# Optimization experiments

Hardware: AMD Instinct MI355X
Metric: run time of the kernel (lower is better)

The kernel has to match this reference:

```python
import jax, jax.numpy as jnp
import numpy as np

H = 128
STEPS = 4
EPS = 1e-5

def _mlp(x, W0, b0, W1, b1, W2, b2):
    x = jax.nn.relu(x @ W0 + b0)
    x = jax.nn.relu(x @ W1 + b1)
    return x @ W2 + b2

def _ln(x, g, b):
    mu = jnp.mean(x, axis=-1, keepdims=True)
    var = jnp.mean((x - mu) ** 2, axis=-1, keepdims=True)
    return (x - mu) * jax.lax.rsqrt(var + EPS) * g + b

def _scores(x, pos):
    # soft assignment of points to graph nodes: softmax over -squared distance
    d2 = (jnp.sum(x * x, -1, keepdims=True)
          - 2.0 * jnp.einsum('bnd,md->bnm', x, pos)
          + jnp.sum(pos * pos, -1))  # [B, Npts, Nnodes]
    return jax.nn.softmax(-d2, axis=-1)

def _block(nodes, senders, receivers, msg_W, msg_b, ln1_g, ln1_b, node_W, node_b, ln2_g, ln2_b):
    # gather edge endpoints, message MLP, layernorm
    m = jnp.concatenate((nodes[:, receivers], nodes[:, senders]), axis=-1) @ msg_W + msg_b
    m = _ln(m, ln1_g, ln1_b)  # [B, E, H]
    inbox = jnp.zeros_like(nodes).at[:, receivers].add(m)  # scatter-add
    out = jnp.concatenate((nodes, inbox), axis=-1) @ node_W + node_b
    return _ln(out, ln2_g, ln2_b)

def setup_inputs() -> dict:
    key = jax.random.key(0)
    ks = jax.random.split(key, 40)
    B, Nc, Nt, N, E = 8, 4096, 4096, 1024, 16384
    dx, dyc, dyt = 2, 3, 3
    def w(k, *s):
        fan_in = s[0]
        return jax.random.normal(k, s, jnp.float32) / np.sqrt(fan_in)
    inp = {
        'xc': jax.random.normal(ks[0], (B, Nc, dx), jnp.float32),
        'yc': jax.random.normal(ks[1], (B, Nc, dyc), jnp.float32),
        'xt': jax.random.normal(ks[2], (B, Nt, dx), jnp.float32),
        'pos': jax.random.normal(ks[3], (N, dx), jnp.float32),
        'enc_W0': w(ks[4], dx + dyc, H), 'enc_b0': jnp.zeros((H,), jnp.float32),
        'enc_W1': w(ks[5], H, H), 'enc_b1': jnp.zeros((H,), jnp.float32),
        'enc_W2': w(ks[6], H, H), 'enc_b2': jnp.zeros((H,), jnp.float32),
        'qenc_W0': w(ks[7], dx, H), 'qenc_b0': jnp.zeros((H,), jnp.float32),
        'qenc_W1': w(ks[8], H, H), 'qenc_b1': jnp.zeros((H,), jnp.float32),
        'qenc_W2': w(ks[9], H, H), 'qenc_b2': jnp.zeros((H,), jnp.float32),
        'dec_W0': w(ks[10], 2 * H, H), 'dec_b0': jnp.zeros((H,), jnp.float32),
        'dec_W1': w(ks[11], H, H), 'dec_b1': jnp.zeros((H,), jnp.float32),
        'dec_W2': w(ks[12], H, dyt), 'dec_b2': jnp.zeros((dyt,), jnp.float32),
        'msg_W': w(ks[13], 2 * H, H), 'msg_b': jnp.zeros((H,), jnp.float32),
        'ln1_g': jnp.ones((H,), jnp.float32), 'ln1_b': jnp.zeros((H,), jnp.float32),
        'node_W': w(ks[14], 2 * H, H), 'node_b': jnp.zeros((H,), jnp.float32),
        'ln2_g': jnp.ones((H,), jnp.float32), 'ln2_b': jnp.zeros((H,), jnp.float32),
        'senders': jax.random.randint(ks[15], (E,), 0, N, jnp.int32),
        'receivers': jax.random.randint(ks[16], (E,), 0, N, jnp.int32),
    }
    return inp

def reference(xc, yc, xt, pos,
              enc_W0, enc_b0, enc_W1, enc_b1, enc_W2, enc_b2,
              qenc_W0, qenc_b0, qenc_W1, qenc_b1, qenc_W2, qenc_b2,
              dec_W0, dec_b0, dec_W1, dec_b1, dec_W2, dec_b2,
              msg_W, msg_b, ln1_g, ln1_b, node_W, node_b, ln2_g, ln2_b,
              senders, receivers):
    sc = _scores(xc, pos)  # [B, Nc, N]
    emb = _mlp(jnp.concatenate((xc, yc), -1), enc_W0, enc_b0, enc_W1, enc_b1, enc_W2, enc_b2)
    latents = jnp.einsum('bcn,bch->bnh', sc, emb)  # scores^T @ emb -> [B, N, H]
    for _ in range(STEPS):  # shared block (same weights each step)
        latents = _block(latents, senders, receivers, msg_W, msg_b, ln1_g, ln1_b,
                         node_W, node_b, ln2_g, ln2_b)
    q = _mlp(xt, qenc_W0, qenc_b0, qenc_W1, qenc_b1, qenc_W2, qenc_b2)
    st = _scores(xt, pos)  # [B, Nt, N]
    z = jnp.einsum('btn,bnh->bth', st, latents)
    z = jnp.concatenate((z, q), -1)
    return _mlp(z, dec_W0, dec_b0, dec_W1, dec_b1, dec_W2, dec_b2)
```

## Files before the change

kernel.cpp:

```cpp
#include <hip/hip_runtime.h>
#include <hip/hip_bf16.h>
#include <string.h>

#define BB 8
#define NC 4096
#define NTT 4096
#define NNODE 1024
#define NEDGE 16384
#define LDE 4128
#define LDL 1056

typedef __hip_bfloat16 bf16;
typedef unsigned short u16;
typedef __attribute__((ext_vector_type(8))) short short8;
typedef __attribute__((ext_vector_type(4))) float f32x4;

__device__ __forceinline__ float b2f(bf16 x) { return __bfloat162float(x); }
__device__ __forceinline__ float bs2f(short s) { return __uint_as_float(((unsigned)(unsigned short)s) << 16); }

template <typename T> struct Cvt;
template <> struct Cvt<float> { static __device__ __forceinline__ float to(float v) { return v; } };
template <> struct Cvt<bf16>  { static __device__ __forceinline__ bf16  to(float v) { return __float2bfloat16(v); } };

__device__ __forceinline__ unsigned short f2bs(float x) {
    unsigned u = __float_as_uint(x);
    return (unsigned short)((u + 0x7FFFu + ((u >> 16) & 1u)) >> 16);
}

__device__ __forceinline__ short8 ld_frag(const bf16* g) {
    union { uint4 u4; short8 s8; } cv;
    cv.u4 = *(const uint4*)g;
    return cv.s8;
}
__device__ __forceinline__ short8 ld_frag(const float* g) {
    float4 f0 = *(const float4*)g;
    float4 f1 = *(const float4*)(g + 4);
    short8 r;
    r[0] = (short)f2bs(f0.x); r[1] = (short)f2bs(f0.y);
    r[2] = (short)f2bs(f0.z); r[3] = (short)f2bs(f0.w);
    r[4] = (short)f2bs(f1.x); r[5] = (short)f2bs(f1.y);
    r[6] = (short)f2bs(f1.z); r[7] = (short)f2bs(f1.w);
    return r;
}

__global__ void detect_k(const u16* __restrict__ posu, int* __restrict__ flag) {
    __shared__ int cnt;
    if (threadIdx.x == 0) cnt = 0;
    __syncthreads();
    int wild = 0;
    for (int i = threadIdx.x; i < 1024; i += 256) {
        u16 u = posu[2 * i];
        int ex = (u >> 7) & 0xFF;
        if (ex == 0 || ex == 0xFF || ex > 137 || ex < 107) wild++;
    }
    atomicAdd(&cnt, wild);
    __syncthreads();
    if (threadIdx.x == 0) *flag = (cnt > 50) ? 1 : 0;
}

struct Tab { const void* src[30]; int pref[31]; };

__global__ __launch_bounds__(256) void ingest_k(Tab tab, const int* __restrict__ flag,
                                                bf16* __restrict__ dst) {
    int idx = blockIdx.x * 256 + threadIdx.x;
    if (idx >= tab.pref[30]) return;
    int t = 0;
    while (tab.pref[t + 1] <= idx) t++;
    int e = idx - tab.pref[t];
    float v;
    if (*flag) v = ((const float*)tab.src[t])[e];
    else       v = b2f(((const bf16*)tab.src[t])[e]);
    dst[idx] = __float2bfloat16(v);
}

struct TT { const bf16* src[11]; bf16* dst[11]; int srcK[11]; int dK[11]; int pref[12]; };

__global__ __launch_bounds__(256) void prep_trans_k(
    TT tt,
    const bf16* __restrict__ xc, const bf16* __restrict__ yc,
    const bf16* __restrict__ xt,
    const bf16* __restrict__ pos,
    bf16* __restrict__ xin32, bf16* __restrict__ xt32,
    float2* __restrict__ posf2) {
    if (blockIdx.x < 128) {
        int row = blockIdx.x * 256 + threadIdx.x;
        bf16 z = __float2bfloat16(0.f);
        bf16* xr = xin32 + row * 32;
        xr[0] = xc[row * 2 + 0];
        xr[1] = xc[row * 2 + 1];
        xr[2] = yc[row * 3 + 0];
        xr[3] = yc[row * 3 + 1];
        xr[4] = yc[row * 3 + 2];
#pragma unroll
        for (int k = 5; k < 32; ++k) xr[k] = z;
        bf16* tr = xt32 + row * 32;
        tr[0] = xt[row * 2 + 0];
        tr[1] = xt[row * 2 + 1];
#pragma unroll
        for (int k = 2; k < 32; ++k) tr[k] = z;
        if (row < NNODE) posf2[row] = make_float2(b2f(pos[2 * row]), b2f(pos[2 * row + 1]));
        return;
    }
    int idx = (blockIdx.x - 128) * 256 + threadIdx.x;
    if (idx >= tt.pref[11]) return;
    int t = 0;
    while (tt.pref[t + 1] <= idx) t++;
    int e = idx - tt.pref[t];
    int k = e >> 7, n = e & 127;
    bf16 v = (k < tt.srcK[t]) ? tt.src[t][k * 128 + n] : __float2bfloat16(0.f);
    tt.dst[t][n * tt.dK[t] + k] = v;
}

__global__ __launch_bounds__(1024) void build_csr_k(const int* __restrict__ recv,
                                                    const int* __restrict__ send,
                                                    int* __restrict__ rowptr,
                                                    int* __restrict__ csr_send) {
    __shared__ int cnt[1024];
    __shared__ int wt[16], wt2[16];
    __shared__ int cur[1024];
    int t = threadIdx.x;
    cnt[t] = 0;
    __syncthreads();
    for (int e = t; e < NEDGE; e += 1024) atomicAdd(&cnt[recv[e]], 1);
    __syncthreads();
    int v = cnt[t];
    int lane = t & 63, w = t >> 6;
#pragma unroll
    for (int off = 1; off < 64; off <<= 1) {
        int u = __shfl_up(v, off);
        if (lane >= off) v += u;
    }
    if (lane == 63) wt[w] = v;
    __syncthreads();
    if (t < 16) {
        int x = wt[t];
#pragma unroll
        for (int off = 1; off < 16; off <<= 1) {
            int u = __shfl_up(x, off);
            if (t >= off) x += u;
        }
        wt2[t] = x;
    }
    __syncthreads();
    int excl = v - cnt[t] + (w ? wt2[w - 1] : 0);
    rowptr[t] = excl;
    cur[t] = excl;
    if (t == 0) rowptr[1024] = NEDGE;
    __syncthreads();
    for (int e = t; e < NEDGE; e += 1024) {
        int pos = atomicAdd(&cur[recv[e]], 1);
        csr_send[pos] = send[e];
    }
}

template <int KSTEPS, int EPI, int RELU, int TRANS, int NSPLIT,
          typename TINA, typename TINB, typename TOUT>
__global__ __launch_bounds__(256) void mfma_gemm_k(
    const TINA* __restrict__ Xa, const TINB* __restrict__ Xb, int ldx,
    const bf16* __restrict__ Wt,
    const bf16* __restrict__ bias,
    const bf16* __restrict__ lng, const bf16* __restrict__ lnb,
    TOUT* __restrict__ Y, int ldy, int tshift, int ldt)
{
    constexpr int K = KSTEPS * 32;
    __shared__ __align__(16) short Bs[8][64][8];
    int tid = threadIdx.x;
    int w = tid >> 6, l = tid & 63;
    int lm = l & 15, lq = l >> 4;
    int blk = blockIdx.x;
    int half = 0;
    if (NSPLIT == 2) { half = blk & 1; blk >>= 1; }
    const bf16* Wtl = Wt + (size_t)half * 128 * K;
    int colbase = half * 128;
    size_t row0 = (size_t)blk * 64;

    f32x4 acc[8];
#pragma unroll
    for (int i = 0; i < 8; i++) acc[i] = (f32x4){0.f, 0.f, 0.f, 0.f};

    for (int s = 0; s < KSTEPS; ++s) {
        int k0 = s * 32;
        __syncthreads();
        short8 a;
        if (Xb != nullptr && k0 >= 128)
            a = ld_frag(Xb + (row0 + w * 16 + lm) * (size_t)128 + (k0 - 128) + lq * 8);
        else
            a = ld_frag(Xa + (row0 + w * 16 + lm) * (size_t)ldx + k0 + lq * 8);
#pragma unroll
        for (int rr = 0; rr < 2; ++rr) {
            int idx = rr * 256 + tid;
            int nt = idx >> 6, ll = idx & 63;
            *(short8*)&Bs[nt][ll][0] =
                ld_frag(Wtl + (size_t)(nt * 16 + (ll & 15)) * K + k0 + (ll >> 4) * 8);
        }
        __syncthreads();
#pragma unroll
        for (int nt = 0; nt < 8; ++nt) {
            short8 b = *(const short8*)&Bs[nt][l][0];
            acc[nt] = __builtin_amdgcn_mfma_f32_16x16x32_bf16(a, b, acc[nt], 0, 0, 0);
        }
    }

    float v[8][4];
#pragma unroll
    for (int nt = 0; nt < 8; ++nt) {
        float bb = bias ? b2f(bias[colbase + nt * 16 + lm]) : 0.f;
#pragma unroll
        for (int r = 0; r < 4; ++r) v[nt][r] = acc[nt][r] + bb;
    }
    if constexpr (EPI == 1) {
#pragma unroll
        for (int r = 0; r < 4; ++r) {
            float s1 = 0.f, s2 = 0.f;
#pragma unroll
            for (int nt = 0; nt < 8; ++nt) { s1 += v[nt][r]; s2 += v[nt][r] * v[nt][r]; }
#pragma unroll
            for (int m = 1; m < 16; m <<= 1) { s1 += __shfl_xor(s1, m); s2 += __shfl_xor(s2, m); }
            float mu = s1 * (1.f / 128.f);
            float var = s2 * (1.f / 128.f) - mu * mu;
            float rs = rsqrtf(var + 1e-5f);
#pragma unroll
            for (int nt = 0; nt < 8; ++nt) {
                int n = nt * 16 + lm;
                v[nt][r] = (v[nt][r] - mu) * rs * b2f(lng[n]) + b2f(lnb[n]);
            }
        }
    }
    if constexpr (TRANS) {
        size_t grow = row0 + w * 16 + lq * 4;
        int bb2 = (int)(grow >> tshift);
        size_t rloc = grow & (((size_t)1 << tshift) - 1);
        bf16* YT = (bf16*)Y;
#pragma unroll
        for (int nt = 0; nt < 8; ++nt) {
            int col = colbase + nt * 16 + lm;
            ushort4 u;
            float x0 = v[nt][0], x1 = v[nt][1], x2 = v[nt][2], x3 = v[nt][3];
            if (RELU) { x0 = fmaxf(x0, 0.f); x1 = fmaxf(x1, 0.f); x2 = fmaxf(x2, 0.f); x3 = fmaxf(x3, 0.f); }
            u.x = f2bs(x0); u.y = f2bs(x1); u.z = f2bs(x2); u.w = f2bs(x3);
            *(ushort4*)(YT + ((size_t)bb2 * 128 + col) * (size_t)ldt + rloc) = u;
        }
    } else {
#pragma unroll
        for (int nt = 0; nt < 8; ++nt)
#pragma unroll
            for (int r = 0; r < 4; ++r) {
                float x = v[nt][r];
                if (RELU) x = fmaxf(x, 0.f);
                Y[(row0 + w * 16 + lq * 4 + r) * (size_t)ldy + colbase + nt * 16 + lm] = Cvt<TOUT>::to(x);
            }
    }
}

__global__ __launch_bounds__(256) void node_msg_k(
    const float* __restrict__ cur, const bf16* __restrict__ inbox,
    const bf16* __restrict__ WtNode, const bf16* __restrict__ node_b,
    const bf16* __restrict__ ln2_g, const bf16* __restrict__ ln2_b,
    const bf16* __restrict__ WtMsg,
    float* __restrict__ nxt, bf16* __restrict__ PQ)
{
    __shared__ __align__(16) short Bs[8][64][8];
    __shared__ __align__(16) short Act[64][136];
    int tid = threadIdx.x;
    int w = tid >> 6, l = tid & 63;
    int lm = l & 15, lq = l >> 4;
    size_t row0 = (size_t)blockIdx.x * 64;

    f32x4 acc[8];
#pragma unroll
    for (int i = 0; i < 8; i++) acc[i] = (f32x4){0.f, 0.f, 0.f, 0.f};

    for (int s = 0; s < 8; ++s) {
        int k0 = s * 32;
        __syncthreads();
        short8 a;
        if (k0 < 128) a = ld_frag(cur + (row0 + w * 16 + lm) * 128 + k0 + lq * 8);
        else          a = ld_frag(inbox + (row0 + w * 16 + lm) * 128 + (k0 - 128) + lq * 8);
#pragma unroll
        for (int rr = 0; rr < 2; ++rr) {
            int idx = rr * 256 + tid;
            int nt = idx >> 6, ll = idx & 63;
            *(short8*)&Bs[nt][ll][0] =
                ld_frag(WtNode + (size_t)(nt * 16 + (ll & 15)) * 256 + k0 + (ll >> 4) * 8);
        }
        __syncthreads();
#pragma unroll
        for (int nt = 0; nt < 8; ++nt) {
            short8 b = *(const short8*)&Bs[nt][l][0];
            acc[nt] = __builtin_amdgcn_mfma_f32_16x16x32_bf16(a, b, acc[nt], 0, 0, 0);
        }
    }
    float v[8][4];
#pragma unroll
    for (int nt = 0; nt < 8; ++nt) {
        float bb = b2f(node_b[nt * 16 + lm]);
#pragma unroll
        for (int r = 0; r < 4; ++r) v[nt][r] = acc[nt][r] + bb;
    }
#pragma unroll
    for (int r = 0; r < 4; ++r) {
        float s1 = 0.f, s2 = 0.f;
#pragma unroll
        for (int nt = 0; nt < 8; ++nt) { s1 += v[nt][r]; s2 += v[nt][r] * v[nt][r]; }
#pragma unroll
        for (int m = 1; m < 16; m <<= 1) { s1 += __shfl_xor(s1, m); s2 += __shfl_xor(s2, m); }
        float mu = s1 * (1.f / 128.f);
        float var = s2 * (1.f / 128.f) - mu * mu;
        float rs = rsqrtf(var + 1e-5f);
#pragma unroll
        for (int nt = 0; nt < 8; ++nt) {
            int n = nt * 16 + lm;
            v[nt][r] = (v[nt][r] - mu) * rs * b2f(ln2_g[n]) + b2f(ln2_b[n]);
        }
    }
#pragma unroll
    for (int nt = 0; nt < 8; ++nt)
#pragma unroll
        for (int r = 0; r < 4; ++r) {
            nxt[(row0 + w * 16 + lq * 4 + r) * 128 + nt * 16 + lm] = v[nt][r];
            Act[w * 16 + lq * 4 + r][nt * 16 + lm] = (short)f2bs(v[nt][r]);
        }

    for (int half = 0; half < 2; ++half) {
        const bf16* Wtl = WtMsg + (size_t)half * 128 * 128;
#pragma unroll
        for (int i = 0; i < 8; i++) acc[i] = (f32x4){0.f, 0.f, 0.f, 0.f};
        for (int s = 0; s < 4; ++s) {
            int k0 = s * 32;
            __syncthreads();
#pragma unroll
            for (int rr = 0; rr < 2; ++rr) {
                int idx = rr * 256 + tid;
                int nt = idx >> 6, ll = idx & 63;
                *(short8*)&Bs[nt][ll][0] =
                    ld_frag(Wtl + (size_t)(nt * 16 + (ll & 15)) * 128 + k0 + (ll >> 4) * 8);
            }
            __syncthreads();
            short8 a = *(const short8*)&Act[w * 16 + lm][k0 + lq * 8];
#pragma unroll
            for (int nt = 0; nt < 8; ++nt) {
                short8 b = *(const short8*)&Bs[nt][l][0];
                acc[nt] = __builtin_amdgcn_mfma_f32_16x16x32_bf16(a, b, acc[nt], 0, 0, 0);
            }
        }
#pragma unroll
        for (int nt = 0; nt < 8; ++nt)
#pragma unroll
            for (int r = 0; r < 4; ++r)
                PQ[(row0 + w * 16 + lq * 4 + r) * 256 + half * 128 + nt * 16 + lm] =
                    __float2bfloat16(acc[nt][r]);
    }
}

template <int K0STEPS, int LAYERS, int RELU_LAST, int TRANS, typename TIN, typename TOUT>
__global__ __launch_bounds__(256) void mlp_k(
    const TIN* __restrict__ Xa, const TIN* __restrict__ Xb, int ldx,
    const bf16* __restrict__ Wt0, const bf16* __restrict__ b0,
    const bf16* __restrict__ Wt1, const bf16* __restrict__ b1,
    const bf16* __restrict__ Wt2, const bf16* __restrict__ b2,
    TOUT* __restrict__ Y, int ldy, int tshift, int ldt)
{
    constexpr int K0 = K0STEPS * 32;
    __shared__ __align__(16) short Bs[8][64][8];
    __shared__ __align__(16) short Act[64][136];
    int tid = threadIdx.x;
    int w = tid >> 6, l = tid & 63;
    int lm = l & 15, lq = l >> 4;
    size_t row0 = (size_t)blockIdx.x * 64;

    f32x4 acc[8];
#pragma unroll
    for (int i = 0; i < 8; i++) acc[i] = (f32x4){0.f, 0.f, 0.f, 0.f};

    for (int s = 0; s < K0STEPS; ++s) {
        int k0 = s * 32;
        __syncthreads();
        short8 a;
        {
            const TIN* src = Xa; int kk = k0; int ld = ldx;
            if (Xb != nullptr && k0 >= 128) { src = Xb; kk = k0 - 128; ld = 128; }
            a = ld_frag(src + (row0 + w * 16 + lm) * (size_t)ld + kk + lq * 8);
        }
#pragma unroll
        for (int rr = 0; rr < 2; ++rr) {
            int idx = rr * 256 + tid;
            int nt = idx >> 6, ll = idx & 63;
            *(short8*)&Bs[nt][ll][0] =
                ld_frag(Wt0 + (size_t)(nt * 16 + (ll & 15)) * K0 + k0 + (ll >> 4) * 8);
        }
        __syncthreads();
#pragma unroll
        for (int nt = 0; nt < 8; ++nt) {
            short8 b = *(const short8*)&Bs[nt][l][0];
            acc[nt] = __builtin_amdgcn_mfma_f32_16x16x32_bf16(a, b, acc[nt], 0, 0, 0);
        }
    }
#pragma unroll
    for (int nt = 0; nt < 8; ++nt) {
        float bb = b2f(b0[nt * 16 + lm]);
#pragma unroll
        for (int r = 0; r < 4; ++r) {
            float x = fmaxf(acc[nt][r] + bb, 0.f);
            Act[w * 16 + lq * 4 + r][nt * 16 + lm] = (short)f2bs(x);
        }
    }

    for (int L = 1; L < LAYERS; ++L) {
        const bf16* Wt = (L == 1) ? Wt1 : Wt2;
        const bf16* bias = (L == 1) ? b1 : b2;
        bool last = (L == LAYERS - 1);
#pragma unroll
        for (int i = 0; i < 8; i++) acc[i] = (f32x4){0.f, 0.f, 0.f, 0.f};
        for (int s = 0; s < 4; ++s) {
            int k0 = s * 32;
            __syncthreads();
#pragma unroll
            for (int rr = 0; rr < 2; ++rr) {
                int idx = rr * 256 + tid;
                int nt = idx >> 6, ll = idx & 63;
                *(short8*)&Bs[nt][ll][0] =
                    ld_frag(Wt + (size_t)(nt * 16 + (ll & 15)) * 128 + k0 + (ll >> 4) * 8);
            }
            __syncthreads();
            short8 a = *(const short8*)&Act[w * 16 + lm][k0 + lq * 8];
#pragma unroll
            for (int nt = 0; nt < 8; ++nt) {
                short8 b = *(const short8*)&Bs[nt][l][0];
                acc[nt] = __builtin_amdgcn_mfma_f32_16x16x32_bf16(a, b, acc[nt], 0, 0, 0);
            }
        }
        if (!last) {
            __syncthreads();
#pragma unroll
            for (int nt = 0; nt < 8; ++nt) {
                float bb = b2f(bias[nt * 16 + lm]);
#pragma unroll
                for (int r = 0; r < 4; ++r) {
                    float x = fmaxf(acc[nt][r] + bb, 0.f);
                    Act[w * 16 + lq * 4 + r][nt * 16 + lm] = (short)f2bs(x);
                }
            }
        } else {
            float v[8][4];
#pragma unroll
            for (int nt = 0; nt < 8; ++nt) {
                float bb = b2f(bias[nt * 16 + lm]);
#pragma unroll
                for (int r = 0; r < 4; ++r) {
                    float x = acc[nt][r] + bb;
                    if (RELU_LAST) x = fmaxf(x, 0.f);
                    v[nt][r] = x;
                }
            }
            if constexpr (TRANS) {
                size_t grow = row0 + w * 16 + lq * 4;
                int bb2 = (int)(grow >> tshift);
                size_t rloc = grow & (((size_t)1 << tshift) - 1);
                bf16* YT = (bf16*)Y;
#pragma unroll
                for (int nt = 0; nt < 8; ++nt) {
                    int col = nt * 16 + lm;
                    ushort4 u;
                    u.x = f2bs(v[nt][0]); u.y = f2bs(v[nt][1]);
                    u.z = f2bs(v[nt][2]); u.w = f2bs(v[nt][3]);
                    *(ushort4*)(YT + ((size_t)bb2 * 128 + col) * (size_t)ldt + rloc) = u;
                }
            } else {
#pragma unroll
                for (int nt = 0; nt < 8; ++nt)
#pragma unroll
                    for (int r = 0; r < 4; ++r)
                        Y[(row0 + w * 16 + lq * 4 + r) * (size_t)ldy + nt * 16 + lm] =
                            Cvt<TOUT>::to(v[nt][r]);
            }
        }
    }
}

__global__ __launch_bounds__(256) void qdec_k(
    const bf16* __restrict__ xt32,
    const bf16* __restrict__ WtQ0, const bf16* __restrict__ qb0,
    const bf16* __restrict__ WtQ1, const bf16* __restrict__ qb1,
    const bf16* __restrict__ WtQ2, const bf16* __restrict__ qb2,
    const bf16* __restrict__ z,
    const bf16* __restrict__ WtDec0, const bf16* __restrict__ db0,
    const bf16* __restrict__ WtDec1, const bf16* __restrict__ db1,
    const bf16* __restrict__ W2, const bf16* __restrict__ b2v,
    const int* __restrict__ flag, void* __restrict__ out)
{
    __shared__ __align__(16) short Bs[8][64][8];
    __shared__ __align__(16) short Act[64][136];
    __shared__ bf16 w2s[384];
    int tid = threadIdx.x;
    int w = tid >> 6, l = tid & 63;
    int lm = l & 15, lq = l >> 4;
    size_t row0 = (size_t)blockIdx.x * 64;
    for (int t = tid; t < 384; t += 256) w2s[t] = W2[t];

    f32x4 acc[8];
#pragma unroll
    for (int i = 0; i < 8; i++) acc[i] = (f32x4){0.f, 0.f, 0.f, 0.f};

    {
        __syncthreads();
#pragma unroll
        for (int rr = 0; rr < 2; ++rr) {
            int idx = rr * 256 + tid;
            int nt = idx >> 6, ll = idx & 63;
            *(short8*)&Bs[nt][ll][0] =
                ld_frag(WtQ0 + (size_t)(nt * 16 + (ll & 15)) * 32 + (ll >> 4) * 8);
        }
        __syncthreads();
        short8 a = ld_frag(xt32 + (row0 + w * 16 + lm) * 32 + lq * 8);
#pragma unroll
        for (int nt = 0; nt < 8; ++nt) {
            short8 b = *(const short8*)&Bs[nt][l][0];
            acc[nt] = __builtin_amdgcn_mfma_f32_16x16x32_bf16(a, b, acc[nt], 0, 0, 0);
        }
#pragma unroll
        for (int nt = 0; nt < 8; ++nt) {
            float bb = b2f(qb0[nt * 16 + lm]);
#pragma unroll
            for (int r = 0; r < 4; ++r)
                Act[w * 16 + lq * 4 + r][nt * 16 + lm] = (short)f2bs(fmaxf(acc[nt][r] + bb, 0.f));
        }
    }
    for (int L = 1; L < 3; ++L) {
        const bf16* Wt = (L == 1) ? WtQ1 : WtQ2;
        const bf16* bias = (L == 1) ? qb1 : qb2;
#pragma unroll
        for (int i = 0; i < 8; i++) acc[i] = (f32x4){0.f, 0.f, 0.f, 0.f};
        for (int s = 0; s < 4; ++s) {
            int k0 = s * 32;
            __syncthreads();
#pragma unroll
            for (int rr = 0; rr < 2; ++rr) {
                int idx = rr * 256 + tid;
                int nt = idx >> 6, ll = idx & 63;
                *(short8*)&Bs[nt][ll][0] =
                    ld_frag(Wt + (size_t)(nt * 16 + (ll & 15)) * 128 + k0 + (ll >> 4) * 8);
            }
            __syncthreads();
            short8 a = *(const short8*)&Act[w * 16 + lm][k0 + lq * 8];
#pragma unroll
            for (int nt = 0; nt < 8; ++nt) {
                short8 b = *(const short8*)&Bs[nt][l][0];
                acc[nt] = __builtin_amdgcn_mfma_f32_16x16x32_bf16(a, b, acc[nt], 0, 0, 0);
            }
        }
        __syncthreads();
#pragma unroll
        for (int nt = 0; nt < 8; ++nt) {
            float bb = b2f(bias[nt * 16 + lm]);
#pragma unroll
            for (int r = 0; r < 4; ++r) {
                float x = acc[nt][r] + bb;
                if (L == 1) x = fmaxf(x, 0.f);
                Act[w * 16 + lq * 4 + r][nt * 16 + lm] = (short)f2bs(x);
            }
        }
    }
    {
#pragma unroll
        for (int i = 0; i < 8; i++) acc[i] = (f32x4){0.f, 0.f, 0.f, 0.f};
        for (int s = 0; s < 8; ++s) {
            int k0 = s * 32;
            __syncthreads();
#pragma unroll
            for (int rr = 0; rr < 2; ++rr) {
                int idx = rr * 256 + tid;
                int nt = idx >> 6, ll = idx & 63;
                *(short8*)&Bs[nt][ll][0] =
                    ld_frag(WtDec0 + (size_t)(nt * 16 + (ll & 15)) * 256 + k0 + (ll >> 4) * 8);
            }
            __syncthreads();
            short8 a;
            if (k0 < 128) a = ld_frag(z + (row0 + w * 16 + lm) * (size_t)128 + k0 + lq * 8);
            else          a = *(const short8*)&Act[w * 16 + lm][(k0 - 128) + lq * 8];
#pragma unroll
            for (int nt = 0; nt < 8; ++nt) {
                short8 b = *(const short8*)&Bs[nt][l][0];
                acc[nt] = __builtin_amdgcn_mfma_f32_16x16x32_bf16(a, b, acc[nt], 0, 0, 0);
            }
        }
        __syncthreads();
#pragma unroll
        for (int nt = 0; nt < 8; ++nt) {
            float bb = b2f(db0[nt * 16 + lm]);
#pragma unroll
            for (int r = 0; r < 4; ++r)
                Act[w * 16 + lq * 4 + r][nt * 16 + lm] = (short)f2bs(fmaxf(acc[nt][r] + bb, 0.f));
        }
    }
    {
#pragma unroll
        for (int i = 0; i < 8; i++) acc[i] = (f32x4){0.f, 0.f, 0.f, 0.f};
        for (int s = 0; s < 4; ++s) {
            int k0 = s * 32;
            __syncthreads();
#pragma unroll
            for (int rr = 0; rr < 2; ++rr) {
                int idx = rr * 256 + tid;
                int nt = idx >> 6, ll = idx & 63;
                *(short8*)&Bs[nt][ll][0] =
                    ld_frag(WtDec1 + (size_t)(nt * 16 + (ll & 15)) * 128 + k0 + (ll >> 4) * 8);
            }
            __syncthreads();
            short8 a = *(const short8*)&Act[w * 16 + lm][k0 + lq * 8];
#pragma unroll
            for (int nt = 0; nt < 8; ++nt) {
                short8 b = *(const short8*)&Bs[nt][l][0];
                acc[nt] = __builtin_amdgcn_mfma_f32_16x16x32_bf16(a, b, acc[nt], 0, 0, 0);
            }
        }
        __syncthreads();
#pragma unroll
        for (int nt = 0; nt < 8; ++nt) {
            float bb = b2f(db1[nt * 16 + lm]);
#pragma unroll
            for (int r = 0; r < 4; ++r)
                Act[w * 16 + lq * 4 + r][nt * 16 + lm] = (short)f2bs(fmaxf(acc[nt][r] + bb, 0.f));
        }
    }
    __syncthreads();
    if (tid < 192) {
        int row = tid / 3, col = tid - (tid / 3) * 3;
        float a = b2f(b2v[col]);
        for (int k8 = 0; k8 < 16; ++k8) {
            short8 av = *(const short8*)&Act[row][k8 * 8];
#pragma unroll
            for (int j = 0; j < 8; ++j)
                a += bs2f(av[j]) * b2f(w2s[(k8 * 8 + j) * 3 + col]);
        }
        size_t o = (row0 + row) * 3 + col;
        if (*flag) ((float*)out)[o] = a;
        else       ((bf16*)out)[o] = __float2bfloat16(a);
    }
}

__global__ __launch_bounds__(256) void stats2_k(const bf16* __restrict__ xcp,
                                                const bf16* __restrict__ xtp,
                                                const bf16* __restrict__ pos,
                                                float4* __restrict__ cstC4,
                                                float4* __restrict__ cstT4) {
    __shared__ float px[NNODE], py[NNODE];
    int tid = threadIdx.x;
    for (int t = tid; t < NNODE; t += 256) {
        px[t] = b2f(pos[2 * t]);
        py[t] = b2f(pos[2 * t + 1]);
    }
    __syncthreads();
    const bf16* xp = (blockIdx.x < 8192) ? xcp : xtp;
    float4* st4 = (blockIdx.x < 8192) ? cstC4 : cstT4;
    int pb = blockIdx.x & 8191;
    int w = tid >> 6, l = tid & 63;
    int p = pb * 4 + w;
    float x = b2f(xp[2 * p]), y = b2f(xp[2 * p + 1]);
    float vals[16];
    float m = -3.4e38f;
#pragma unroll
    for (int k = 0; k < 16; k++) {
        int n = k * 64 + l;
        float dx = x - px[n], dy = y - py[n];
        float v = -(dx * dx + dy * dy);
        vals[k] = v;
        m = fmaxf(m, v);
    }
#pragma unroll
    for (int off = 32; off; off >>= 1) m = fmaxf(m, __shfl_xor(m, off));
    float s = 0.f;
#pragma unroll
    for (int k = 0; k < 16; k++) s += __expf(vals[k] - m);
#pragma unroll
    for (int off = 32; off; off >>= 1) s += __shfl_xor(s, off);
    if (l == 0) st4[p] = make_float4(x, y, m, 1.f / s);
}

struct P8 { float* p[8]; };

__global__ __launch_bounds__(512, 4) void lat_mfma_k(const bf16* __restrict__ embT,
                                                     const float2* __restrict__ posf2,
                                                     const float4* __restrict__ cstC4,
                                                     P8 parts) {
    int i = blockIdx.x;
    int b = i & 7, r = i >> 3;
    int cs = r >> 4, nt = r & 15;
    int n0 = nt * 64;
    __shared__ __align__(16) float4 csh[512];
    __shared__ __align__(16) union ShU {
        short stage[2][8192];
        float4 red[4][8][64];
    } sh;
    int tid = threadIdx.x;
    int w = tid >> 6, l = tid & 63;
    int wl = w & 3, up = w >> 2;
    int lm = l & 15, lq = l >> 4;
    int node = n0 + wl * 16 + lm;
    float2 pn = posf2[node];
    const bf16* ebase = embT + (size_t)b * (128 * LDE) + cs * 512;
    const float4* cbase = cstC4 + b * NC + cs * 512;
    csh[tid] = cbase[tid];

    int h0 = tid >> 3;
    int cb0 = (tid & 7) << 4;
    const char* g0 = (const char*)ebase + (size_t)h0 * (LDE * 2) + cb0;
    const size_t gH = (size_t)64 * (LDE * 2);
    int o0 = h0 * 128 + (cb0 ^ ((h0 & 7) << 4));
    char* lbuf0 = (char*)&sh.stage[0][0];
    char* lbuf1 = (char*)&sh.stage[1][0];

    {
        uint4 rA = *(const uint4*)(g0);
        uint4 rB = *(const uint4*)(g0 + gH);
        *(uint4*)(lbuf0 + o0) = rA;
        *(uint4*)(lbuf0 + o0 + 64 * 128) = rB;
    }
    __syncthreads();

    f32x4 acc[8];
#pragma unroll
    for (int q = 0; q < 8; q++) acc[q] = (f32x4){0.f, 0.f, 0.f, 0.f};

    union AF { short8 s; u16 u[8]; };
    int rb = up * 64 + lq * 16;

    for (int ci = 0; ci < 8; ++ci) {
        char* cur = (ci & 1) ? lbuf1 : lbuf0;
        char* nxt = (ci & 1) ? lbuf0 : lbuf1;
        uint4 rA, rB;
        if (ci < 7) {
            const char* gs = g0 + (ci + 1) * 128;
            rA = *(const uint4*)(gs);
            rB = *(const uint4*)(gs + gH);
        }
        AF cw;
        int cidx = ci * 64 + up * 32 + lq * 8;
#pragma unroll
        for (int j = 0; j < 8; ++j) {
            float4 cc = csh[cidx + j];
            float dx = cc.x - pn.x, dy = cc.y - pn.y;
            cw.u[j] = f2bs(__expf(-(dx * dx + dy * dy) - cc.z) * cc.w);
        }
#pragma unroll
        for (int t2 = 0; t2 < 8; ++t2) {
            int h = t2 * 16 + lm;
            short8 bfr = *(const short8*)(cur + h * 128 + (rb ^ ((h & 7) << 4)));
            acc[t2] = __builtin_amdgcn_mfma_f32_16x16x32_bf16(cw.s, bfr, acc[t2], 0, 0, 0);
        }
        if (ci < 7) {
            *(uint4*)(nxt + o0) = rA;
            *(uint4*)(nxt + o0 + 64 * 128) = rB;
        }
        __syncthreads();
    }

    if (up) {
#pragma unroll
        for (int t2 = 0; t2 < 8; ++t2)
            sh.red[wl][t2][l] = make_float4(acc[t2][0], acc[t2][1], acc[t2][2], acc[t2][3]);
    }
    __syncthreads();
    if (!up) {
        float* part = parts.p[cs] + (((size_t)(b * NNODE + n0 + wl * 16 + lq * 4)) << 7) + lm;
#pragma unroll
        for (int t2 = 0; t2 < 8; ++t2) {
            float4 o = sh.red[wl][t2][l];
#pragma unroll
            for (int r2 = 0; r2 < 4; ++r2)
                part[(r2 << 7) + t2 * 16] = acc[t2][r2] + ((const float*)&o)[r2];
        }
    }
}

__global__ __launch_bounds__(256) void reduce8_k(float* __restrict__ dst, P8 parts) {
    int i = blockIdx.x * 256 + threadIdx.x;
    float4 s = ((const float4*)parts.p[0])[i];
#pragma unroll
    for (int k = 1; k < 8; ++k) {
        float4 v = ((const float4*)parts.p[k])[i];
        s.x += v.x; s.y += v.y; s.z += v.z; s.w += v.w;
    }
    ((float4*)dst)[i] = s;
}

__global__ __launch_bounds__(512, 4) void z_mfma_k(const bf16* __restrict__ latT,
                                                   const float2* __restrict__ posf2,
                                                   const float4* __restrict__ cstT4,
                                                   bf16* __restrict__ z) {
    int i = blockIdx.x;
    int b = i & 7, tt = i >> 3;
    int t0 = tt * 64;
    __shared__ __align__(8) float2 posh[1024];
    __shared__ __align__(16) union ShU {
        short stage[2][8192];
        float4 red[4][8][64];
    } sh;
    int tid = threadIdx.x;
    int w = tid >> 6, l = tid & 63;
    int wl = w & 3, up = w >> 2;
    int lm = l & 15, lq = l >> 4;
    int t = t0 + wl * 16 + lm;
    float4 qs = cstT4[b * NTT + t];
    const bf16* lbase = latT + (size_t)b * (128 * LDL);
    for (int k = tid; k < 1024; k += 512) posh[k] = posf2[k];

    int h0 = tid >> 3;
    int cb0 = (tid & 7) << 4;
    const char* g0 = (const char*)lbase + (size_t)h0 * (LDL * 2) + cb0;
    const size_t gH = (size_t)64 * (LDL * 2);
    int o0 = h0 * 128 + (cb0 ^ ((h0 & 7) << 4));
    char* lbuf0 = (char*)&sh.stage[0][0];
    char* lbuf1 = (char*)&sh.stage[1][0];

    {
        uint4 rA = *(const uint4*)(g0);
        uint4 rB = *(const uint4*)(g0 + gH);
        *(uint4*)(lbuf0 + o0) = rA;
        *(uint4*)(lbuf0 + o0 + 64 * 128) = rB;
    }
    __syncthreads();

    f32x4 acc[8];
#pragma unroll
    for (int q = 0; q < 8; q++) acc[q] = (f32x4){0.f, 0.f, 0.f, 0.f};

    union AF { short8 s; u16 u[8]; };
    int rb = up * 64 + lq * 16;

    for (int ci = 0; ci < 16; ++ci) {
        char* cur = (ci & 1) ? lbuf1 : lbuf0;
        char* nxt = (ci & 1) ? lbuf0 : lbuf1;
        uint4 rA, rB;
        if (ci < 15) {
            const char* gs = g0 + (ci + 1) * 128;
            rA = *(const uint4*)(gs);
            rB = *(const uint4*)(gs + gH);
        }
        AF cw;
        int cidx = ci * 64 + up * 32 + lq * 8;
#pragma unroll
        for (int j = 0; j < 8; ++j) {
            float2 pn = posh[cidx + j];
            float dx = qs.x - pn.x, dy = qs.y - pn.y;
            cw.u[j] = f2bs(__expf(-(dx * dx + dy * dy) - qs.z) * qs.w);
        }
#pragma unroll
        for (int t2 = 0; t2 < 8; ++t2) {
            int h = t2 * 16 + lm;
            short8 bfr = *(const short8*)(cur + h * 128 + (rb ^ ((h & 7) << 4)));
            acc[t2] = __builtin_amdgcn_mfma_f32_16x16x32_bf16(cw.s, bfr, acc[t2], 0, 0, 0);
        }
        if (ci < 15) {
            *(uint4*)(nxt + o0) = rA;
            *(uint4*)(nxt + o0 + 64 * 128) = rB;
        }
        __syncthreads();
    }

    if (up) {
#pragma unroll
        for (int t2 = 0; t2 < 8; ++t2)
            sh.red[wl][t2][l] = make_float4(acc[t2][0], acc[t2][1], acc[t2][2], acc[t2][3]);
    }
    __syncthreads();
    if (!up) {
        bf16* zp = z + (((size_t)(b * NTT + t0 + wl * 16 + lq * 4)) << 7) + lm;
#pragma unroll
        for (int t2 = 0; t2 < 8; ++t2) {
            float4 o = sh.red[wl][t2][l];
#pragma unroll
            for (int r2 = 0; r2 < 4; ++r2)
                zp[(r2 << 7) + t2 * 16] = __float2bfloat16(acc[t2][r2] + ((const float*)&o)[r2]);
        }
    }
}

__global__ __launch_bounds__(256) void edge_gather_k(const bf16* __restrict__ PQ,
                                                     const int* __restrict__ rowptr,
                                                     const int* __restrict__ csr_send,
                                                     const bf16* __restrict__ mb,
                                                     const bf16* __restrict__ g1,
                                                     const bf16* __restrict__ b1,
                                                     bf16* __restrict__ inbox) {
    int tid = threadIdx.x;
    int w = tid >> 6, l = tid & 63;
    int gw = blockIdx.x * 4 + w;
    int b = gw >> 10, n = gw & 1023;
    const bf16* pqb = PQ + ((size_t)b << 18);
    float p0 = b2f(pqb[(n << 8) + l]);
    float p1 = b2f(pqb[(n << 8) + l + 64]);
    float mb0 = b2f(mb[l]), mb1 = b2f(mb[l + 64]);
    float g0 = b2f(g1[l]), g1v = b2f(g1[l + 64]);
    float bb0 = b2f(b1[l]), bb1 = b2f(b1[l + 64]);
    int beg = rowptr[n], end = rowptr[n + 1];
    float a0 = 0.f, a1 = 0.f;
    int i = beg;
    for (; i + 1 < end; i += 2) {
        int sA = csr_send[i], sB = csr_send[i + 1];
        const bf16* qA = pqb + (sA << 8) + 128;
        const bf16* qB = pqb + (sB << 8) + 128;
        float A0 = p0 + b2f(qA[l]) + mb0;
        float A1 = p1 + b2f(qA[l + 64]) + mb1;
        float B0 = p0 + b2f(qB[l]) + mb0;
        float B1 = p1 + b2f(qB[l + 64]) + mb1;
        float a1s = A0 + A1, a2s = A0 * A0 + A1 * A1;
        float b1s = B0 + B1, b2s = B0 * B0 + B1 * B1;
#pragma unroll
        for (int off = 32; off; off >>= 1) {
            a1s += __shfl_xor(a1s, off);
            a2s += __shfl_xor(a2s, off);
            b1s += __shfl_xor(b1s, off);
            b2s += __shfl_xor(b2s, off);
        }
        float muA = a1s * (1.f / 128.f);
        float varA = a2s * (1.f / 128.f) - muA * muA;
        float rsA = rsqrtf(varA + 1e-5f);
        float muB = b1s * (1.f / 128.f);
        float varB = b2s * (1.f / 128.f) - muB * muB;
        float rsB = rsqrtf(varB + 1e-5f);
        a0 += (A0 - muA) * rsA * g0 + bb0;
        a1 += (A1 - muA) * rsA * g1v + bb1;
        a0 += (B0 - muB) * rsB * g0 + bb0;
        a1 += (B1 - muB) * rsB * g1v + bb1;
    }
    if (i < end) {
        int s = csr_send[i];
        const bf16* q = pqb + (s << 8) + 128;
        float m0 = p0 + b2f(q[l]) + mb0;
        float m1 = p1 + b2f(q[l + 64]) + mb1;
        float s1 = m0 + m1, s2 = m0 * m0 + m1 * m1;
#pragma unroll
        for (int off = 32; off; off >>= 1) {
            s1 += __shfl_xor(s1, off);
            s2 += __shfl_xor(s2, off);
        }
        float mu = s1 * (1.f / 128.f);
        float var = s2 * (1.f / 128.f) - mu * mu;
        float rs = rsqrtf(var + 1e-5f);
        a0 += (m0 - mu) * rs * g0 + bb0;
        a1 += (m1 - mu) * rs * g1v + bb1;
    }
    bf16* inb = inbox + ((size_t)b << 17) + (n << 7);
    inb[l] = __float2bfloat16(a0);
    inb[l + 64] = __float2bfloat16(a1);
}

extern "C" void kernel_launch(void* const* d_in, const int* in_sizes, int n_in,
                              void* d_out, int out_size, void* d_ws, size_t ws_size,
                              hipStream_t stream) {
    const int* senders = (const int*)d_in[30];
    const int* receivers = (const int*)d_in[31];

    char* base = (char*)d_ws;
    size_t off = 0;
    auto alloc = [&](size_t bytes) { char* p = base + off; off += (bytes + 255) & ~(size_t)255; return p; };

    int* flag = (int*)alloc(256);

    Tab tab;
    int pref = 0;
    for (int i = 0; i < 30; ++i) { tab.src[i] = d_in[i]; tab.pref[i] = pref; pref += in_sizes[i]; }
    tab.pref[30] = pref;
    bf16* arena = (bf16*)alloc((size_t)pref * 2);
    auto C = [&](int i) { return arena + tab.pref[i]; };

    float4* cstC4 = (float4*)alloc(32768 * sizeof(float4));
    float4* cstT4 = (float4*)alloc(32768 * sizeof(float4));
    float* lat0  = (float*)alloc(8192 * 128 * 4);
    float* lat1  = (float*)alloc(8192 * 128 * 4);
    float* inboxf = (float*)alloc(8192 * 128 * 4);
    bf16* inbox  = (bf16*)alloc(8192 * 128 * 2);
    bf16* T1     = (bf16*)alloc((size_t)32768 * 128 * 2);
    bf16* T2     = (bf16*)alloc((size_t)32768 * 128 * 2);
    bf16* T3     = (bf16*)alloc((size_t)32768 * 128 * 2);
    bf16* embT   = (bf16*)alloc((size_t)8 * 128 * LDE * 2);
    bf16* latT   = (bf16*)alloc((size_t)8 * 128 * LDL * 2);
    bf16* xin32  = (bf16*)alloc((size_t)32768 * 32 * 2);
    bf16* xt32   = (bf16*)alloc((size_t)32768 * 32 * 2);
    float2* posf2 = (float2*)alloc(1024 * sizeof(float2));
    int* rowptr  = (int*)alloc(1025 * 4);
    int* csr_send = (int*)alloc(NEDGE * 4);
    bf16* WtEnc0 = (bf16*)alloc(128 * 32 * 2);
    bf16* WtQ0   = (bf16*)alloc(128 * 32 * 2);
    bf16* WtEnc1 = (bf16*)alloc(16384 * 2);
    bf16* WtEnc2 = (bf16*)alloc(16384 * 2);
    bf16* WtQ1   = (bf16*)alloc(16384 * 2);
    bf16* WtQ2   = (bf16*)alloc(16384 * 2);
    bf16* WtDec0 = (bf16*)alloc(32768 * 2);
    bf16* WtDec1 = (bf16*)alloc(16384 * 2);
    bf16* WtMsg  = (bf16*)alloc(32768 * 2);
    bf16* WtNode = (bf16*)alloc(32768 * 2);
    bf16* PQ     = T3;
    (void)ws_size; (void)n_in; (void)out_size;

    detect_k<<<1, 256, 0, stream>>>((const u16*)d_in[3], flag);
    ingest_k<<<(pref + 255) / 256, 256, 0, stream>>>(tab, flag, arena);

    const bf16 *xc = C(0), *yc = C(1), *xt = C(2), *pos = C(3);
    const bf16 *enc_W0 = C(4), *enc_b0 = C(5), *enc_W1 = C(6), *enc_b1 = C(7), *enc_W2 = C(8), *enc_b2 = C(9);
    const bf16 *qenc_W0 = C(10), *qenc_b0 = C(11), *qenc_W1 = C(12), *qenc_b1 = C(13), *qenc_W2 = C(14), *qenc_b2 = C(15);
    const bf16 *dec_W0 = C(16), *dec_b0 = C(17), *dec_W1 = C(18), *dec_b1 = C(19), *dec_W2 = C(20), *dec_b2 = C(21);
    const bf16 *msg_W = C(22), *msg_b = C(23), *ln1_g = C(24), *ln1_b = C(25);
    const bf16 *node_W = C(26), *node_b = C(27), *ln2_g = C(28), *ln2_b = C(29);

    TT tt;
    const bf16* s11[11] = { enc_W1, enc_W2, qenc_W1, qenc_W2, dec_W1, dec_W0, msg_W, msg_W + 16384, node_W, enc_W0, qenc_W0 };
    bf16* d11[11]       = { WtEnc1, WtEnc2, WtQ1,    WtQ2,    WtDec1, WtDec0, WtMsg, WtMsg + 16384, WtNode, WtEnc0, WtQ0   };
    int sk11[11] = { 128, 128, 128, 128, 128, 256, 128, 128, 256, 5, 2 };
    int dk11[11] = { 128, 128, 128, 128, 128, 256, 128, 128, 256, 32, 32 };
    int tp = 0;
    for (int i = 0; i < 11; ++i) {
        tt.src[i] = s11[i]; tt.dst[i] = d11[i]; tt.srcK[i] = sk11[i]; tt.dK[i] = dk11[i];
        tt.pref[i] = tp; tp += dk11[i] * 128;
    }
    tt.pref[11] = tp;

    prep_trans_k<<<128 + (tp + 255) / 256, 256, 0, stream>>>(tt, xc, yc, xt, pos, xin32, xt32, posf2);
    build_csr_k<<<1, 1024, 0, stream>>>(receivers, senders, rowptr, csr_send);

    mlp_k<1, 3, 0, 1, bf16, bf16><<<512, 256, 0, stream>>>(
        xin32, nullptr, 32, WtEnc0, enc_b0, WtEnc1, enc_b1, WtEnc2, enc_b2, embT, 128, 12, LDE);

    stats2_k<<<16384, 256, 0, stream>>>(xc, xt, pos, cstC4, cstT4);

    P8 parts;
    parts.p[0] = lat1;
    parts.p[1] = inboxf;
    parts.p[2] = (float*)T1;
    parts.p[3] = (float*)T1 + 1048576;
    parts.p[4] = (float*)T2;
    parts.p[5] = (float*)T2 + 1048576;
    parts.p[6] = (float*)T3;
    parts.p[7] = (float*)T3 + 1048576;
    lat_mfma_k<<<1024, 512, 0, stream>>>(embT, posf2, cstC4, parts);
    reduce8_k<<<1024, 256, 0, stream>>>(lat0, parts);

    mfma_gemm_k<4, 0, 0, 0, 2, float, float, bf16><<<256, 256, 0, stream>>>(lat0, nullptr, 128, WtMsg, nullptr, nullptr, nullptr, PQ, 256, 0, 0);
    edge_gather_k<<<2048, 256, 0, stream>>>(PQ, rowptr, csr_send, msg_b, ln1_g, ln1_b, inbox);
    node_msg_k<<<128, 256, 0, stream>>>(lat0, inbox, WtNode, node_b, ln2_g, ln2_b, WtMsg, lat1, PQ);
    edge_gather_k<<<2048, 256, 0, stream>>>(PQ, rowptr, csr_send, msg_b, ln1_g, ln1_b, inbox);
    node_msg_k<<<128, 256, 0, stream>>>(lat1, inbox, WtNode, node_b, ln2_g, ln2_b, WtMsg, lat0, PQ);
    edge_gather_k<<<2048, 256, 0, stream>>>(PQ, rowptr, csr_send, msg_b, ln1_g, ln1_b, inbox);
    node_msg_k<<<128, 256, 0, stream>>>(lat0, inbox, WtNode, node_b, ln2_g, ln2_b, WtMsg, lat1, PQ);
    edge_gather_k<<<2048, 256, 0, stream>>>(PQ, rowptr, csr_send, msg_b, ln1_g, ln1_b, inbox);
    mfma_gemm_k<8, 1, 0, 1, 1, float, bf16, bf16><<<128, 256, 0, stream>>>(lat1, inbox, 128, WtNode, node_b, ln2_g, ln2_b, latT, 128, 10, LDL);

    z_mfma_k<<<512, 512, 0, stream>>>(latT, posf2, cstT4, T2);

    qdec_k<<<512, 256, 0, stream>>>(xt32,
                                    WtQ0, qenc_b0, WtQ1, qenc_b1, WtQ2, qenc_b2,
                                    T2,
                                    WtDec0, dec_b0, WtDec1, dec_b1,
                                    dec_W2, dec_b2, flag, d_out);
}
```

Measured before the change: 442.1 us.

## Factor edge layernorm using precomputed sender stats and dot-product decomposition

The GEMM and node kernels that produce the sender half of PQ now also emit per-row mean and sum-of-squares into a small vstat buffer. The edge gather kernel rebuilds each message's layernorm statistics from the receiver's stats, the sender's stats and one receiver-sender dot product. It accumulates scalar sums (R, M, t0, t1) and applies gamma and beta once per node instead of once per edge. This halves the wave reductions per edge and removes per-edge normalization arithmetic. The cost is an extra global read per edge and possibly worse numerics from the expanded variance formula.

```diff
diff --git a/kernel.cpp b/kernel.cpp
--- a/kernel.cpp
+++ b/kernel.cpp
@@ -160,7 +160,8 @@
     const bf16* __restrict__ Wt,
     const bf16* __restrict__ bias,
     const bf16* __restrict__ lng, const bf16* __restrict__ lnb,
-    TOUT* __restrict__ Y, int ldy, int tshift, int ldt)
+    TOUT* __restrict__ Y, int ldy, int tshift, int ldt,
+    float2* __restrict__ vstat)
 {
     constexpr int K = KSTEPS * 32;
     __shared__ __align__(16) short Bs[8][64][8];
@@ -249,6 +250,21 @@
                 if (RELU) x = fmaxf(x, 0.f);
                 Y[(row0 + w * 16 + lq * 4 + r) * (size_t)ldy + colbase + nt * 16 + lm] = Cvt<TOUT>::to(x);
             }
+        if (vstat != nullptr && half == 1) {
+#pragma unroll
+            for (int r = 0; r < 4; ++r) {
+                float s1 = 0.f, s2 = 0.f;
+#pragma unroll
+                for (int nt = 0; nt < 8; ++nt) {
+                    float vv = bs2f((short)f2bs(v[nt][r]));
+                    s1 += vv; s2 += vv * vv;
+                }
+#pragma unroll
+                for (int m = 1; m < 16; m <<= 1) { s1 += __shfl_xor(s1, m); s2 += __shfl_xor(s2, m); }
+                if (lm == 0)
+                    vstat[row0 + w * 16 + lq * 4 + r] = make_float2(s1 * (1.f / 128.f), s2);
+            }
+        }
     }
 }
 
@@ -257,7 +273,8 @@
     const bf16* __restrict__ WtNode, const bf16* __restrict__ node_b,
     const bf16* __restrict__ ln2_g, const bf16* __restrict__ ln2_b,
     const bf16* __restrict__ WtMsg,
-    float* __restrict__ nxt, bf16* __restrict__ PQ)
+    float* __restrict__ nxt, bf16* __restrict__ PQ,
+    float2* __restrict__ vstat)
 {
     __shared__ __align__(16) short Bs[8][64][8];
     __shared__ __align__(16) short Act[64][136];
@@ -349,6 +366,21 @@
             for (int r = 0; r < 4; ++r)
                 PQ[(row0 + w * 16 + lq * 4 + r) * 256 + half * 128 + nt * 16 + lm] =
                     __float2bfloat16(acc[nt][r]);
+        if (half == 1) {
+#pragma unroll
+            for (int r = 0; r < 4; ++r) {
+                float s1 = 0.f, s2 = 0.f;
+#pragma unroll
+                for (int nt = 0; nt < 8; ++nt) {
+                    float vv = bs2f((short)f2bs(acc[nt][r]));
+                    s1 += vv; s2 += vv * vv;
+                }
+#pragma unroll
+                for (int m = 1; m < 16; m <<= 1) { s1 += __shfl_xor(s1, m); s2 += __shfl_xor(s2, m); }
+                if (lm == 0)
+                    vstat[row0 + w * 16 + lq * 4 + r] = make_float2(s1 * (1.f / 128.f), s2);
+            }
+        }
     }
 }
 
@@ -876,6 +908,7 @@
 }
 
 __global__ __launch_bounds__(256) void edge_gather_k(const bf16* __restrict__ PQ,
+                                                     const float2* __restrict__ vstat,
                                                      const int* __restrict__ rowptr,
                                                      const int* __restrict__ csr_send,
                                                      const bf16* __restrict__ mb,
@@ -887,59 +920,67 @@
     int gw = blockIdx.x * 4 + w;
     int b = gw >> 10, n = gw & 1023;
     const bf16* pqb = PQ + ((size_t)b << 18);
-    float p0 = b2f(pqb[(n << 8) + l]);
-    float p1 = b2f(pqb[(n << 8) + l + 64]);
-    float mb0 = b2f(mb[l]), mb1 = b2f(mb[l + 64]);
+    const float2* vsb = vstat + b * NNODE;
+    float u0 = b2f(pqb[(n << 8) + l]) + b2f(mb[l]);
+    float u1 = b2f(pqb[(n << 8) + l + 64]) + b2f(mb[l + 64]);
     float g0 = b2f(g1[l]), g1v = b2f(g1[l + 64]);
     float bb0 = b2f(b1[l]), bb1 = b2f(b1[l + 64]);
+    float s1 = u0 + u1, s2 = u0 * u0 + u1 * u1;
+#pragma unroll
+    for (int off = 32; off; off >>= 1) {
+        s1 += __shfl_xor(s1, off);
+        s2 += __shfl_xor(s2, off);
+    }
+    float aN = s1 * (1.f / 128.f);
+    float Su = s2;
     int beg = rowptr[n], end = rowptr[n + 1];
-    float a0 = 0.f, a1 = 0.f;
+    float R = 0.f, M = 0.f, t0 = 0.f, t1 = 0.f;
     int i = beg;
     for (; i + 1 < end; i += 2) {
         int sA = csr_send[i], sB = csr_send[i + 1];
         const bf16* qA = pqb + (sA << 8) + 128;
         const bf16* qB = pqb + (sB << 8) + 128;
-        float A0 = p0 + b2f(qA[l]) + mb0;
-        float A1 = p1 + b2f(qA[l + 64]) + mb1;
-        float B0 = p0 + b2f(qB[l]) + mb0;
-        float B1 = p1 + b2f(qB[l + 64]) + mb1;
-        float a1s = A0 + A1, a2s = A0 * A0 + A1 * A1;
-        float b1s = B0 + B1, b2s = B0 * B0 + B1 * B1;
+        float vA0 = b2f(qA[l]), vA1 = b2f(qA[l + 64]);
+        float vB0 = b2f(qB[l]), vB1 = b2f(qB[l + 64]);
+        float dA = u0 * vA0 + u1 * vA1;
+        float dB = u0 * vB0 + u1 * vB1;
 #pragma unroll
         for (int off = 32; off; off >>= 1) {
-            a1s += __shfl_xor(a1s, off);
-            a2s += __shfl_xor(a2s, off);
-            b1s += __shfl_xor(b1s, off);
-            b2s += __shfl_xor(b2s, off);
-        }
-        float muA = a1s * (1.f / 128.f);
-        float varA = a2s * (1.f / 128.f) - muA * muA;
+            dA += __shfl_xor(dA, off);
+            dB += __shfl_xor(dB, off);
+        }
+        float2 stA = vsb[sA];
+        float2 stB = vsb[sB];
+        float muA = aN + stA.x;
+        float varA = (Su + stA.y + 2.f * dA) * (1.f / 128.f) - muA * muA;
         float rsA = rsqrtf(varA + 1e-5f);
-        float muB = b1s * (1.f / 128.f);
-        float varB = b2s * (1.f / 128.f) - muB * muB;
+        float muB = aN + stB.x;
+        float varB = (Su + stB.y + 2.f * dB) * (1.f / 128.f) - muB * muB;
         float rsB = rsqrtf(varB + 1e-5f);
-        a0 += (A0 - muA) * rsA * g0 + bb0;
-        a1 += (A1 - muA) * rsA * g1v + bb1;
-        a0 += (B0 - muB) * rsB * g0 + bb0;
-        a1 += (B1 - muB) * rsB * g1v + bb1;
+        R += rsA + rsB;
+        M += rsA * muA + rsB * muB;
+        t0 += rsA * vA0 + rsB * vB0;
+        t1 += rsA * vA1 + rsB * vB1;
     }
     if (i < end) {
         int s = csr_send[i];
         const bf16* q = pqb + (s << 8) + 128;
-        float m0 = p0 + b2f(q[l]) + mb0;
-        float m1 = p1 + b2f(q[l + 64]) + mb1;
-        float s1 = m0 + m1, s2 = m0 * m0 + m1 * m1;
-#pragma unroll
-        for (int off = 32; off; off >>= 1) {
-            s1 += __shfl_xor(s1, off);
-            s2 += __shfl_xor(s2, off);
-        }
-        float mu = s1 * (1.f / 128.f);
-        float var = s2 * (1.f / 128.f) - mu * mu;
+        float v0 = b2f(q[l]), v1 = b2f(q[l + 64]);
+        float d = u0 * v0 + u1 * v1;
+#pragma unroll
+        for (int off = 32; off; off >>= 1) d += __shfl_xor(d, off);
+        float2 st = vsb[s];
+        float mu = aN + st.x;
+        float var = (Su + st.y + 2.f * d) * (1.f / 128.f) - mu * mu;
         float rs = rsqrtf(var + 1e-5f);
-        a0 += (m0 - mu) * rs * g0 + bb0;
-        a1 += (m1 - mu) * rs * g1v + bb1;
-    }
+        R += rs;
+        M += rs * mu;
+        t0 += rs * v0;
+        t1 += rs * v1;
+    }
+    float deg = (float)(end - beg);
+    float a0 = g0 * (u0 * R + t0 - M) + deg * bb0;
+    float a1 = g1v * (u1 * R + t1 - M) + deg * bb1;
     bf16* inb = inbox + ((size_t)b << 17) + (n << 7);
     inb[l] = __float2bfloat16(a0);
     inb[l + 64] = __float2bfloat16(a1);
@@ -978,6 +1019,7 @@
     bf16* xin32  = (bf16*)alloc((size_t)32768 * 32 * 2);
     bf16* xt32   = (bf16*)alloc((size_t)32768 * 32 * 2);
     float2* posf2 = (float2*)alloc(1024 * sizeof(float2));
+    float2* vstat = (float2*)alloc(8192 * sizeof(float2));
     int* rowptr  = (int*)alloc(1025 * 4);
     int* csr_send = (int*)alloc(NEDGE * 4);
     bf16* WtEnc0 = (bf16*)alloc(128 * 32 * 2);
@@ -1035,15 +1077,15 @@
     lat_mfma_k<<<1024, 512, 0, stream>>>(embT, posf2, cstC4, parts);
     reduce8_k<<<1024, 256, 0, stream>>>(lat0, parts);
 
-    mfma_gemm_k<4, 0, 0, 0, 2, float, float, bf16><<<256, 256, 0, stream>>>(lat0, nullptr, 128, WtMsg, nullptr, nullptr, nullptr, PQ, 256, 0, 0);
-    edge_gather_k<<<2048, 256, 0, stream>>>(PQ, rowptr, csr_send, msg_b, ln1_g, ln1_b, inbox);
-    node_msg_k<<<128, 256, 0, stream>>>(lat0, inbox, WtNode, node_b, ln2_g, ln2_b, WtMsg, lat1, PQ);
-    edge_gather_k<<<2048, 256, 0, stream>>>(PQ, rowptr, csr_send, msg_b, ln1_g, ln1_b, inbox);
-    node_msg_k<<<128, 256, 0, stream>>>(lat1, inbox, WtNode, node_b, ln2_g, ln2_b, WtMsg, lat0, PQ);
-    edge_gather_k<<<2048, 256, 0, stream>>>(PQ, rowptr, csr_send, msg_b, ln1_g, ln1_b, inbox);
-    node_msg_k<<<128, 256, 0, stream>>>(lat0, inbox, WtNode, node_b, ln2_g, ln2_b, WtMsg, lat1, PQ);
-    edge_gather_k<<<2048, 256, 0, stream>>>(PQ, rowptr, csr_send, msg_b, ln1_g, ln1_b, inbox);
-    mfma_gemm_k<8, 1, 0, 1, 1, float, bf16, bf16><<<128, 256, 0, stream>>>(lat1, inbox, 128, WtNode, node_b, ln2_g, ln2_b, latT, 128, 10, LDL);
+    mfma_gemm_k<4, 0, 0, 0, 2, float, float, bf16><<<256, 256, 0, stream>>>(lat0, nullptr, 128, WtMsg, nullptr, nullptr, nullptr, PQ, 256, 0, 0, vstat);
+    edge_gather_k<<<2048, 256, 0, stream>>>(PQ, vstat, rowptr, csr_send, msg_b, ln1_g, ln1_b, inbox);
+    node_msg_k<<<128, 256, 0, stream>>>(lat0, inbox, WtNode, node_b, ln2_g, ln2_b, WtMsg, lat1, PQ, vstat);
+    edge_gather_k<<<2048, 256, 0, stream>>>(PQ, vstat, rowptr, csr_send, msg_b, ln1_g, ln1_b, inbox);
+    node_msg_k<<<128, 256, 0, stream>>>(lat1, inbox, WtNode, node_b, ln2_g, ln2_b, WtMsg, lat0, PQ, vstat);
+    edge_gather_k<<<2048, 256, 0, stream>>>(PQ, vstat, rowptr, csr_send, msg_b, ln1_g, ln1_b, inbox);
+    node_msg_k<<<128, 256, 0, stream>>>(lat0, inbox, WtNode, node_b, ln2_g, ln2_b, WtMsg, lat1, PQ, vstat);
+    edge_gather_k<<<2048, 256, 0, stream>>>(PQ, vstat, rowptr, csr_send, msg_b, ln1_g, ln1_b, inbox);
+    mfma_gemm_k<8, 1, 0, 1, 1, float, bf16, bf16><<<128, 256, 0, stream>>>(lat1, inbox, 128, WtNode, node_b, ln2_g, ln2_b, latT, 128, 10, LDL, nullptr);
 
     z_mfma_k<<<512, 512, 0, stream>>>(latT, posf2, cstT4, T2);
 
```

After: 410.4 us. 1.08x faster.
